# Performance work log

Hardware: AMD Instinct MI355X
Metric: run time of the kernel (lower is better)

## Reference

```python
import jax, jax.numpy as jnp
import numpy as np
from functools import partial

H = 128  # GRU hidden size
L = 16   # dim_latents


def _gru_dir(x_tbd, W_ih, W_hh, b_ih, b_hh):
    """Single-direction GRU over time-major input x_tbd [T,B,D] -> [T,B,H].
    Torch gate order: r, z, n."""
    T, B, _ = x_tbd.shape
    # Precompute input projections for all timesteps: [T,B,3H]
    xp = jnp.einsum('tbd,gd->tbg', x_tbd, W_ih) + b_ih
    h0 = jnp.zeros((B, H), dtype=x_tbd.dtype)

    def step(h, xp_t):
        gh = h @ W_hh.T + b_hh            # [B,3H]
        xr, xz, xn = jnp.split(xp_t, 3, axis=-1)
        hr, hz, hn = jnp.split(gh, 3, axis=-1)
        r = jax.nn.sigmoid(xr + hr)
        z = jax.nn.sigmoid(xz + hz)
        n = jnp.tanh(xn + r * hn)
        h_new = (1.0 - z) * n + z * h
        return h_new, h_new

    _, ys = jax.lax.scan(step, h0, xp)
    return ys  # [T,B,H]


def setup_inputs() -> dict:
    key = jax.random.key(0)
    ks = jax.random.split(key, 8)
    B, T, N = 256, 1000, 256
    s_ih = 1.0 / np.sqrt(N)
    s_hh = 1.0 / np.sqrt(H)
    s_fc = 1.0 / np.sqrt(2 * H + L)
    return {
        'y_aux': jax.random.normal(ks[0], (B, T, N), dtype=jnp.float32),
        'W_ih_fwd': jax.random.normal(ks[1], (3 * H, N), dtype=jnp.float32) * s_ih,
        'W_hh_fwd': jax.random.normal(ks[2], (3 * H, H), dtype=jnp.float32) * s_hh,
        'b_ih_fwd': jnp.zeros((3 * H,), dtype=jnp.float32),
        'b_hh_fwd': jnp.zeros((3 * H,), dtype=jnp.float32),
        'W_ih_bwd': jax.random.normal(ks[3], (3 * H, N), dtype=jnp.float32) * s_ih,
        'W_hh_bwd': jax.random.normal(ks[4], (3 * H, H), dtype=jnp.float32) * s_hh,
        'b_ih_bwd': jnp.zeros((3 * H,), dtype=jnp.float32),
        'b_hh_bwd': jnp.zeros((3 * H,), dtype=jnp.float32),
        'W_mu': jax.random.normal(ks[5], (L, 2 * H + L), dtype=jnp.float32) * s_fc,
        'b_mu': jnp.zeros((L,), dtype=jnp.float32),
        'W_lv': jax.random.normal(ks[6], (L, 2 * H + L), dtype=jnp.float32) * s_fc,
        'b_lv': jnp.zeros((L,), dtype=jnp.float32),
    }


def reference(y_aux, W_ih_fwd, W_hh_fwd, b_ih_fwd, b_hh_fwd,
              W_ih_bwd, W_hh_bwd, b_ih_bwd, b_hh_bwd,
              W_mu, b_mu, W_lv, b_lv):
    # [B,T,N] -> time-major [T,B,N]
    x = jnp.transpose(y_aux, (1, 0, 2))
    out_f = _gru_dir(x, W_ih_fwd, W_hh_fwd, b_ih_fwd, b_hh_fwd)
    out_b = _gru_dir(x[::-1], W_ih_bwd, W_hh_bwd, b_ih_bwd, b_hh_bwd)[::-1]
    rnn_output = jnp.concatenate([out_f, out_b], axis=-1)  # [T,B,2H]
    # hn[0]: bidirectional hidden states at t=0
    hn0 = rnn_output[0]                                    # [B,2H]
    B = hn0.shape[0]
    temp = jnp.concatenate([jnp.zeros((B, L), dtype=hn0.dtype), hn0], axis=1)
    mu_0 = temp @ W_mu.T + b_mu
    log_var_0 = temp @ W_lv.T + b_lv
    return (mu_0, log_var_0, rnn_output)
```

## Files before the change

### kernel.cpp

```cpp
#include <hip/hip_runtime.h>
#include <hip/hip_bf16.h>

typedef short bf16x8 __attribute__((ext_vector_type(8)));
typedef float f32x4  __attribute__((ext_vector_type(4)));

#define TSTEPS 1000
#define BATCH  256
#define NIN    256
#define HID    128
#define TC     40
#define LOG2E  1.44269504088896f

#define GIDX_N 8192
#define XP4_ELEMS (2ull*TSTEPS*GIDX_N)
#define XP2_OFF_BYTES (XP4_ELEMS*16ull)
#define XP_NEED (XP4_ELEMS*16ull + 2ull*TSTEPS*GIDX_N*8ull)

__device__ __forceinline__ ushort f2bf(float f){
  union { float f; unsigned u; } v; v.f = f;
  unsigned r = v.u + 0x7fffu + ((v.u >> 16) & 1u);
  return (ushort)(r >> 16);
}
__device__ __forceinline__ uint pk2(float lo, float hi){
  __hip_bfloat162 h = __float22bfloat162_rn(make_float2(lo, hi));
  union { __hip_bfloat162 h; uint u; } c; c.h = h; return c.u;
}
__device__ __forceinline__ float bflo(uint w){ union{uint u;float f;}c; c.u = w<<16; return c.f; }
__device__ __forceinline__ float bfhi(uint w){ union{uint u;float f;}c; c.u = w & 0xffff0000u; return c.f; }

__device__ __forceinline__ float sigmoid_fast(float x){
  return __builtin_amdgcn_rcpf(1.f + __expf(-x));
}
__device__ __forceinline__ float tanh_fast(float a){
  const float e = __expf(2.f*fabsf(a));
  const float t = fmaf(-2.f, __builtin_amdgcn_rcpf(e + 1.f), 1.f);
  return copysignf(t, a);
}
__device__ __forceinline__ bf16x8 ld_w8(const float* p){
  union { uint u[4]; bf16x8 v; } c;
  c.u[0]=pk2(p[0],p[1]); c.u[1]=pk2(p[2],p[3]);
  c.u[2]=pk2(p[4],p[5]); c.u[3]=pk2(p[6],p[7]);
  return c.v;
}
__device__ __forceinline__ bf16x8 ld_w8s(const float* p, float s){
  union { uint u[4]; bf16x8 v; } c;
  c.u[0]=pk2(p[0]*s,p[1]*s); c.u[1]=pk2(p[2]*s,p[3]*s);
  c.u[2]=pk2(p[4]*s,p[5]*s); c.u[3]=pk2(p[6]*s,p[7]*s);
  return c.v;
}

__global__ __launch_bounds__(512) void xp_gemm(
    const float* __restrict__ y_aux,
    const float* __restrict__ Wf, const float* __restrict__ bihf, const float* __restrict__ bhhf,
    const float* __restrict__ Wb, const float* __restrict__ bihb, const float* __restrict__ bhhb,
    uint4* __restrict__ xp4, uint2* __restrict__ xp2)
{
  const int nch = TSTEPS/TC;
  const int blk = blockIdx.x;
  const int dir = blk / (16*nch);
  const int rem = blk % (16*nch);
  const int btile = rem / nch;
  const int tch = rem % nch;
  const int b0 = btile*16;
  const int tid=threadIdx.x, wave=tid>>6, lane=tid&63, lrow=lane&15, lgrp=lane>>4;
  const float* Wih = dir? Wb : Wf;
  const float* bih = dir? bihb : bihf;
  const float* bhh = dir? bhhb : bhhf;

  __shared__ __align__(16) ushort xsh[2][16][264];

  bf16x8 wf[3][8];
  float biass[3];
  #pragma unroll
  for (int t3=0;t3<3;++t3){
    const int g = t3*128 + wave*16 + lrow;
    #pragma unroll
    for (int kk=0;kk<8;++kk)
      wf[t3][kk] = ld_w8(Wih + g*NIN + kk*32 + lgrp*8);
    biass[t3] = LOG2E * (bih[g] + (t3<2 ? bhh[g] : 0.f));
  }

  const int row = tid>>5, f8 = tid&31;
  const float* xsrc = y_aux + (size_t)(b0+row)*(TSTEPS*NIN) + (size_t)(tch*TC)*NIN + f8*8;
  {
    float4 a = *(const float4*)xsrc;
    float4 b = *(const float4*)(xsrc+4);
    union{uint u[4]; bf16x8 v;} c;
    c.u[0]=pk2(a.x,a.y); c.u[1]=pk2(a.z,a.w); c.u[2]=pk2(b.x,b.y); c.u[3]=pk2(b.z,b.w);
    *(bf16x8*)&xsh[0][row][f8*8] = c.v;
  }
  __syncthreads();

  const size_t gbase = ((size_t)dir*TSTEPS + (size_t)(tch*TC))*GIDX_N
                     + (size_t)((btile*8 + wave)*64 + lane);
  uint4* s4 = xp4 + gbase;
  uint2* s2 = xp2 + gbase;

  for (int k=0;k<TC;++k){
    const int cur=k&1, nxt=cur^1;
    const bool more = (k < TC-1);
    float4 pa, pb;
    if (more){
      const float* p = xsrc + (size_t)(k+1)*NIN;
      pa = *(const float4*)p;
      pb = *(const float4*)(p+4);
    }
    f32x4 a0={0,0,0,0}, a1={0,0,0,0}, a2={0,0,0,0};
    #pragma unroll
    for (int kk=0;kk<8;++kk){
      bf16x8 a = *(const bf16x8*)&xsh[cur][lrow][kk*32 + lgrp*8];
      a0 = __builtin_amdgcn_mfma_f32_16x16x32_bf16(a, wf[0][kk], a0, 0,0,0);
      a1 = __builtin_amdgcn_mfma_f32_16x16x32_bf16(a, wf[1][kk], a1, 0,0,0);
      a2 = __builtin_amdgcn_mfma_f32_16x16x32_bf16(a, wf[2][kk], a2, 0,0,0);
    }
    uint4 o4;
    o4.x = pk2(fmaf(LOG2E,a0[0],biass[0]), fmaf(LOG2E,a0[1],biass[0]));
    o4.y = pk2(fmaf(LOG2E,a0[2],biass[0]), fmaf(LOG2E,a0[3],biass[0]));
    o4.z = pk2(fmaf(LOG2E,a1[0],biass[1]), fmaf(LOG2E,a1[1],biass[1]));
    o4.w = pk2(fmaf(LOG2E,a1[2],biass[1]), fmaf(LOG2E,a1[3],biass[1]));
    uint2 o2;
    o2.x = pk2(fmaf(LOG2E,a2[0],biass[2]), fmaf(LOG2E,a2[1],biass[2]));
    o2.y = pk2(fmaf(LOG2E,a2[2],biass[2]), fmaf(LOG2E,a2[3],biass[2]));
    *s4 = o4;  s4 += GIDX_N;
    *s2 = o2;  s2 += GIDX_N;
    if (more){
      union{uint u[4]; bf16x8 v;} c;
      c.u[0]=pk2(pa.x,pa.y); c.u[1]=pk2(pa.z,pa.w); c.u[2]=pk2(pb.x,pb.y); c.u[3]=pk2(pb.z,pb.w);
      *(bf16x8*)&xsh[nxt][row][f8*8] = c.v;
    }
    asm volatile("s_waitcnt lgkmcnt(0)\n\ts_barrier" ::: "memory");
  }
}

__global__ __launch_bounds__(512) void gru_rec(
    const uint4* __restrict__ xp4, const uint2* __restrict__ xp2,
    const float* __restrict__ Whhf, const float* __restrict__ bhhf,
    const float* __restrict__ Whhb, const float* __restrict__ bhhb,
    float* __restrict__ out)
{
  const int blk=blockIdx.x, dir=blk>>4, btile=blk&15, b0=btile<<4;
  const int tid=threadIdx.x, wave=tid>>6, lane=tid&63, lrow=lane&15, lgrp=lane>>4;
  const float* Whh = dir? Whhb : Whhf;
  const float* bhh = dir? bhhb : bhhf;

  __shared__ __align__(16) ushort hbuf[2][16][136];

  bf16x8 whh[3][4];
  #pragma unroll
  for (int t3=0;t3<3;++t3){
    const int g = t3*128 + wave*16 + lrow;
    #pragma unroll
    for (int kk=0;kk<4;++kk)
      whh[t3][kk] = ld_w8s(Whh + g*HID + kk*32 + lgrp*8, LOG2E);
  }
  const int hcol = wave*16 + lrow;
  const float bh2s = LOG2E * bhh[256 + hcol];

  { ushort* hb=&hbuf[0][0][0]; for (int i=tid;i<16*136;i+=512) hb[i]=0; }

  const int tt0 = dir? (TSTEPS-1):0;
  const long long d4 = dir? -(long long)GIDX_N : (long long)GIDX_N;
  const size_t gbase = ((size_t)dir*TSTEPS + (size_t)tt0)*GIDX_N
                     + (size_t)((btile*8+wave)*64+lane);
  const uint4* q4p = xp4 + gbase;
  const uint2* q2p = xp2 + gbase;
  uint4 q40 = q4p[0], q41 = q4p[d4];
  uint2 q20 = q2p[0], q21 = q2p[d4];
  const uint4* f4 = q4p + 2*d4;
  const uint2* f2 = q2p + 2*d4;

  float* op = out + 8192 + (size_t)tt0*(BATCH*2*HID)
            + (size_t)(b0 + lgrp*4)*(2*HID) + dir*HID + hcol;
  const long long odel = dir? -(long long)(BATCH*2*HID) : (long long)(BATCH*2*HID);

  float hm[4]={0,0,0,0};
  __syncthreads();

  for (int s=0;s<TSTEPS;++s){
    const int cur=s&1, nxt=cur^1;
    uint4 q42 = *f4; f4 += d4;
    uint2 q22 = *f2; f2 += d4;

    f32x4 ar={0,0,0,0}, az={0,0,0,0}, an={0,0,0,0};
    #pragma unroll
    for (int kk=0;kk<4;++kk){
      bf16x8 a = *(const bf16x8*)&hbuf[cur][lrow][kk*32 + lgrp*8];
      ar = __builtin_amdgcn_mfma_f32_16x16x32_bf16(a, whh[0][kk], ar, 0,0,0);
      az = __builtin_amdgcn_mfma_f32_16x16x32_bf16(a, whh[1][kk], az, 0,0,0);
      an = __builtin_amdgcn_mfma_f32_16x16x32_bf16(a, whh[2][kk], an, 0,0,0);
    }

    float hv[4];
    {
      const float xr[4] = {bflo(q40.x),bfhi(q40.x),bflo(q40.y),bfhi(q40.y)};
      const float xz[4] = {bflo(q40.z),bfhi(q40.z),bflo(q40.w),bfhi(q40.w)};
      const float xn[4] = {bflo(q20.x),bfhi(q20.x),bflo(q20.y),bfhi(q20.y)};
      #pragma unroll
      for (int i=0;i<4;++i){
        const float r = __builtin_amdgcn_rcpf(1.f + __builtin_amdgcn_exp2f(-(ar[i]+xr[i])));
        const float z = __builtin_amdgcn_rcpf(1.f + __builtin_amdgcn_exp2f(-(az[i]+xz[i])));
        const float y  = fmaf(r, an[i]+bh2s, xn[i]);
        const float y2 = y + y;
        const float e  = __builtin_amdgcn_exp2f(fabsf(y2));
        const float t  = fmaf(-2.f, __builtin_amdgcn_rcpf(e+1.f), 1.f);
        const float n  = copysignf(t, y);
        hv[i] = fmaf(z, hm[i]-n, n);
        hm[i] = hv[i];
      }
    }
    const uint p01 = pk2(hv[0],hv[1]);
    const uint p23 = pk2(hv[2],hv[3]);
    hbuf[nxt][lgrp*4+0][hcol] = (ushort)p01;
    hbuf[nxt][lgrp*4+1][hcol] = (ushort)(p01>>16);
    hbuf[nxt][lgrp*4+2][hcol] = (ushort)p23;
    hbuf[nxt][lgrp*4+3][hcol] = (ushort)(p23>>16);
    op[0]   = hv[0];
    op[256] = hv[1];
    op[512] = hv[2];
    op[768] = hv[3];
    op += odel;
    q40=q41; q41=q42; q20=q21; q21=q22;
    asm volatile("s_waitcnt lgkmcnt(0)\n\ts_barrier" ::: "memory");
  }
}

__global__ __launch_bounds__(512) void gru_fused(
    const float* __restrict__ y_aux,
    const float* __restrict__ W_ih_f, const float* __restrict__ W_hh_f,
    const float* __restrict__ b_ih_f, const float* __restrict__ b_hh_f,
    const float* __restrict__ W_ih_b, const float* __restrict__ W_hh_b,
    const float* __restrict__ b_ih_b, const float* __restrict__ b_hh_b,
    float* __restrict__ out)
{
  const int blk  = blockIdx.x;
  const int dir  = blk >> 4;
  const int b0   = (blk & 15) << 4;
  const int tid  = threadIdx.x;
  const int wave = tid >> 6;
  const int lane = tid & 63;
  const int lrow = lane & 15;
  const int lgrp = lane >> 4;

  const float* Wih = dir ? W_ih_b : W_ih_f;
  const float* Whh = dir ? W_hh_b : W_hh_f;
  const float* bih = dir ? b_ih_b : b_ih_f;
  const float* bhh = dir ? b_hh_b : b_hh_f;

  __shared__ __align__(16) ushort hbuf[2][16][136];
  __shared__ __align__(16) ushort xbuf[2][16][264];

  bf16x8 wih_f[3][8];
  bf16x8 whh_f[3][4];
  #pragma unroll
  for (int t3 = 0; t3 < 3; ++t3){
    const int g = t3*128 + wave*16 + lrow;
    #pragma unroll
    for (int kk = 0; kk < 8; ++kk) wih_f[t3][kk] = ld_w8(Wih + g*NIN + kk*32 + lgrp*8);
    #pragma unroll
    for (int kk = 0; kk < 4; ++kk) whh_f[t3][kk] = ld_w8(Whh + g*HID + kk*32 + lgrp*8);
  }
  float bihv[3], bhhv[3];
  #pragma unroll
  for (int t3 = 0; t3 < 3; ++t3){
    const int g = t3*128 + wave*16 + lrow;
    bihv[t3] = bih[g];
    bhhv[t3] = bhh[g];
  }

  for (int i = tid; i < 2*16*136; i += 512) ((ushort*)hbuf)[i] = 0;
  {
    const int row = tid >> 5, f8 = tid & 31;
    const int t0  = dir ? (TSTEPS-1) : 0;
    const float* p = y_aux + (size_t)(b0+row)*(TSTEPS*NIN) + (size_t)t0*NIN + f8*8;
    union{uint u[4]; bf16x8 v;} c;
    float4 a = *(const float4*)p; float4 b = *(const float4*)(p+4);
    c.u[0]=pk2(a.x,a.y); c.u[1]=pk2(a.z,a.w); c.u[2]=pk2(b.x,b.y); c.u[3]=pk2(b.z,b.w);
    *(bf16x8*)&xbuf[0][row][f8*8] = c.v;
  }
  __syncthreads();

  float hm[4] = {0.f, 0.f, 0.f, 0.f};
  const int hcol = wave*16 + lrow;
  float* outr = out + 8192;

  for (int s = 0; s < TSTEPS; ++s){
    const int tt  = dir ? (TSTEPS-1-s) : s;
    const int cur = s & 1, nxt = cur ^ 1;
    const int tn   = dir ? (tt-1) : (tt+1);
    const int prow = tid >> 5, pf8 = tid & 31;
    const bool more = (s < TSTEPS-1);
    float4 pa, pb;
    if (more){
      const float* p = y_aux + (size_t)(b0+prow)*(TSTEPS*NIN) + (size_t)tn*NIN + pf8*8;
      pa = *(const float4*)p;
      pb = *(const float4*)(p+4);
    }

    f32x4 a_rh = {0,0,0,0}, a_zh = {0,0,0,0}, a_nh = {0,0,0,0};
    f32x4 a_rx = {0,0,0,0}, a_zx = {0,0,0,0}, a_nx = {0,0,0,0};
    #pragma unroll
    for (int kk = 0; kk < 4; ++kk){
      bf16x8 a = *(const bf16x8*)&hbuf[cur][lrow][kk*32 + lgrp*8];
      a_rh = __builtin_amdgcn_mfma_f32_16x16x32_bf16(a, whh_f[0][kk], a_rh, 0,0,0);
      a_zh = __builtin_amdgcn_mfma_f32_16x16x32_bf16(a, whh_f[1][kk], a_zh, 0,0,0);
      a_nh = __builtin_amdgcn_mfma_f32_16x16x32_bf16(a, whh_f[2][kk], a_nh, 0,0,0);
    }
    #pragma unroll
    for (int kk = 0; kk < 8; ++kk){
      bf16x8 a = *(const bf16x8*)&xbuf[cur][lrow][kk*32 + lgrp*8];
      a_rx = __builtin_amdgcn_mfma_f32_16x16x32_bf16(a, wih_f[0][kk], a_rx, 0,0,0);
      a_zx = __builtin_amdgcn_mfma_f32_16x16x32_bf16(a, wih_f[1][kk], a_zx, 0,0,0);
      a_nx = __builtin_amdgcn_mfma_f32_16x16x32_bf16(a, wih_f[2][kk], a_nx, 0,0,0);
    }

    #pragma unroll
    for (int i = 0; i < 4; ++i){
      const float rp  = a_rh[i] + a_rx[i] + bihv[0] + bhhv[0];
      const float zp  = a_zh[i] + a_zx[i] + bihv[1] + bhhv[1];
      const float hnp = a_nh[i] + bhhv[2];
      const float xnp = a_nx[i] + bihv[2];
      const float r = sigmoid_fast(rp);
      const float z = sigmoid_fast(zp);
      const float n = tanh_fast(fmaf(r, hnp, xnp));
      const float hv = n + z*(hm[i] - n);
      hm[i] = hv;
      outr[(size_t)tt*(BATCH*2*HID) + (size_t)(b0 + lgrp*4 + i)*(2*HID)
           + dir*HID + hcol] = hv;
      hbuf[nxt][lgrp*4 + i][hcol] = f2bf(hv);
    }

    if (more){
      union{uint u[4]; bf16x8 v;} c;
      c.u[0]=pk2(pa.x,pa.y); c.u[1]=pk2(pa.z,pa.w); c.u[2]=pk2(pb.x,pb.y); c.u[3]=pk2(pb.z,pb.w);
      *(bf16x8*)&xbuf[nxt][prow][pf8*8] = c.v;
    }
    __syncthreads();
  }
}

__global__ void heads(const float* __restrict__ out_rnn,
    const float* __restrict__ W_mu, const float* __restrict__ b_mu,
    const float* __restrict__ W_lv, const float* __restrict__ b_lv,
    float* __restrict__ out)
{
  const int oid   = blockIdx.x*256 + threadIdx.x;
  const int which = oid >> 12;
  const int r     = oid & 4095;
  const int b = r >> 4, j = r & 15;
  const float* W    = which ? W_lv : W_mu;
  const float* bias = which ? b_lv : b_mu;
  const float* h = out_rnn + b*256;
  const float* w = W + j*272 + 16;
  float acc = bias[j];
  for (int c = 0; c < 256; c += 4){
    acc += h[c]*w[c] + h[c+1]*w[c+1] + h[c+2]*w[c+2] + h[c+3]*w[c+3];
  }
  out[(which << 12) + r] = acc;
}

extern "C" void kernel_launch(void* const* d_in, const int* in_sizes, int n_in,
                              void* d_out, int out_size, void* d_ws, size_t ws_size,
                              hipStream_t stream)
{
  const float* y    = (const float*)d_in[0];
  const float* Wihf = (const float*)d_in[1];
  const float* Whhf = (const float*)d_in[2];
  const float* bihf = (const float*)d_in[3];
  const float* bhhf = (const float*)d_in[4];
  const float* Wihb = (const float*)d_in[5];
  const float* Whhb = (const float*)d_in[6];
  const float* bihb = (const float*)d_in[7];
  const float* bhhb = (const float*)d_in[8];
  const float* Wmu  = (const float*)d_in[9];
  const float* bmu  = (const float*)d_in[10];
  const float* Wlv  = (const float*)d_in[11];
  const float* blv  = (const float*)d_in[12];
  float* out = (float*)d_out;

  if (ws_size >= (size_t)XP_NEED){
    uint4* xp4 = (uint4*)d_ws;
    uint2* xp2 = (uint2*)((char*)d_ws + XP2_OFF_BYTES);
    xp_gemm<<<dim3(2*16*(TSTEPS/TC)), dim3(512), 0, stream>>>(
        y, Wihf, bihf, bhhf, Wihb, bihb, bhhb, xp4, xp2);
    gru_rec<<<dim3(32), dim3(512), 0, stream>>>(
        xp4, xp2, Whhf, bhhf, Whhb, bhhb, out);
  } else {
    gru_fused<<<dim3(32), dim3(512), 0, stream>>>(
        y, Wihf, Whhf, bihf, bhhf, Wihb, Whhb, bihb, bhhb, out);
  }
  heads<<<dim3(32), dim3(256), 0, stream>>>(out + 8192, Wmu, bmu, Wlv, blv, out);
}
```

Baseline: 958.7 us.

## Split GRU recurrence K dimension across wave pairs with LDS partial-sum exchange

The recurrent kernel now runs 1024 threads per block: each pair of waves splits the 128-wide hidden K dimension in half, exchanges partial MFMA sums through shared memory, and each wave finishes the gate math for two of the four rows. The aim is to halve the serial MFMA chain and the per-lane transcendental work on each timestep, which sit on the latency-bound critical path. The xp buffers are re-laid out so each half-wave pair reads its own two rows. This adds a second barrier and an LDS round trip per step, which may offset the savings.

```diff
diff --git a/kernel.cpp b/kernel.cpp
--- a/kernel.cpp
+++ b/kernel.cpp
@@ -11,10 +11,10 @@
 #define TC     40
 #define LOG2E  1.44269504088896f
 
-#define GIDX_N 8192
-#define XP4_ELEMS (2ull*TSTEPS*GIDX_N)
-#define XP2_OFF_BYTES (XP4_ELEMS*16ull)
-#define XP_NEED (XP4_ELEMS*16ull + 2ull*TSTEPS*GIDX_N*8ull)
+#define GIDX2_N 16384
+#define XPA_ELEMS (2ull*TSTEPS*GIDX2_N)
+#define XPB_OFF_BYTES (XPA_ELEMS*8ull)
+#define XP_NEED (XPA_ELEMS*8ull + XPA_ELEMS*4ull)
 
 __device__ __forceinline__ ushort f2bf(float f){
   union { float f; unsigned u; } v; v.f = f;
@@ -53,7 +53,7 @@
     const float* __restrict__ y_aux,
     const float* __restrict__ Wf, const float* __restrict__ bihf, const float* __restrict__ bhhf,
     const float* __restrict__ Wb, const float* __restrict__ bihb, const float* __restrict__ bhhb,
-    uint4* __restrict__ xp4, uint2* __restrict__ xp2)
+    uint2* __restrict__ xpA, uint* __restrict__ xpB)
 {
   const int nch = TSTEPS/TC;
   const int blk = blockIdx.x;
@@ -91,10 +91,8 @@
   }
   __syncthreads();
 
-  const size_t gbase = ((size_t)dir*TSTEPS + (size_t)(tch*TC))*GIDX_N
-                     + (size_t)((btile*8 + wave)*64 + lane);
-  uint4* s4 = xp4 + gbase;
-  uint2* s2 = xp2 + gbase;
+  size_t sidx = ((size_t)dir*TSTEPS + (size_t)(tch*TC))*GIDX2_N
+              + (size_t)(((btile*8 + wave)*2)*64 + lane);
 
   for (int k=0;k<TC;++k){
     const int cur=k&1, nxt=cur^1;
@@ -113,16 +111,19 @@
       a1 = __builtin_amdgcn_mfma_f32_16x16x32_bf16(a, wf[1][kk], a1, 0,0,0);
       a2 = __builtin_amdgcn_mfma_f32_16x16x32_bf16(a, wf[2][kk], a2, 0,0,0);
     }
-    uint4 o4;
-    o4.x = pk2(fmaf(LOG2E,a0[0],biass[0]), fmaf(LOG2E,a0[1],biass[0]));
-    o4.y = pk2(fmaf(LOG2E,a0[2],biass[0]), fmaf(LOG2E,a0[3],biass[0]));
-    o4.z = pk2(fmaf(LOG2E,a1[0],biass[1]), fmaf(LOG2E,a1[1],biass[1]));
-    o4.w = pk2(fmaf(LOG2E,a1[2],biass[1]), fmaf(LOG2E,a1[3],biass[1]));
-    uint2 o2;
-    o2.x = pk2(fmaf(LOG2E,a2[0],biass[2]), fmaf(LOG2E,a2[1],biass[2]));
-    o2.y = pk2(fmaf(LOG2E,a2[2],biass[2]), fmaf(LOG2E,a2[3],biass[2]));
-    *s4 = o4;  s4 += GIDX_N;
-    *s2 = o2;  s2 += GIDX_N;
+    const float r0=fmaf(LOG2E,a0[0],biass[0]), r1=fmaf(LOG2E,a0[1],biass[0]);
+    const float r2=fmaf(LOG2E,a0[2],biass[0]), r3=fmaf(LOG2E,a0[3],biass[0]);
+    const float z0=fmaf(LOG2E,a1[0],biass[1]), z1=fmaf(LOG2E,a1[1],biass[1]);
+    const float z2=fmaf(LOG2E,a1[2],biass[1]), z3=fmaf(LOG2E,a1[3],biass[1]);
+    const float n0=fmaf(LOG2E,a2[0],biass[2]), n1=fmaf(LOG2E,a2[1],biass[2]);
+    const float n2=fmaf(LOG2E,a2[2],biass[2]), n3=fmaf(LOG2E,a2[3],biass[2]);
+    uint2 qa0; qa0.x = pk2(r0,r1); qa0.y = pk2(z0,z1);
+    uint2 qa1; qa1.x = pk2(r2,r3); qa1.y = pk2(z2,z3);
+    xpA[sidx]    = qa0;
+    xpA[sidx+64] = qa1;
+    xpB[sidx]    = pk2(n0,n1);
+    xpB[sidx+64] = pk2(n2,n3);
+    sidx += GIDX2_N;
     if (more){
       union{uint u[4]; bf16x8 v;} c;
       c.u[0]=pk2(pa.x,pa.y); c.u[1]=pk2(pa.z,pa.w); c.u[2]=pk2(pb.x,pb.y); c.u[3]=pk2(pb.z,pb.w);
@@ -132,94 +133,121 @@
   }
 }
 
-__global__ __launch_bounds__(512) void gru_rec(
-    const uint4* __restrict__ xp4, const uint2* __restrict__ xp2,
+__global__ __launch_bounds__(1024) void gru_rec16(
+    const uint2* __restrict__ xpA, const uint* __restrict__ xpB,
     const float* __restrict__ Whhf, const float* __restrict__ bhhf,
     const float* __restrict__ Whhb, const float* __restrict__ bhhb,
     float* __restrict__ out)
 {
   const int blk=blockIdx.x, dir=blk>>4, btile=blk&15, b0=btile<<4;
   const int tid=threadIdx.x, wave=tid>>6, lane=tid&63, lrow=lane&15, lgrp=lane>>4;
+  const int g = wave>>1, kh = wave&1;
   const float* Whh = dir? Whhb : Whhf;
   const float* bhh = dir? bhhb : bhhf;
 
   __shared__ __align__(16) ushort hbuf[2][16][136];
-
-  bf16x8 whh[3][4];
+  __shared__ __align__(16) float rA[16][64][4];
+  __shared__ __align__(16) float rB[16][64][2];
+
+  bf16x8 whh[3][2];
   #pragma unroll
   for (int t3=0;t3<3;++t3){
-    const int g = t3*128 + wave*16 + lrow;
-    #pragma unroll
-    for (int kk=0;kk<4;++kk)
-      whh[t3][kk] = ld_w8s(Whh + g*HID + kk*32 + lgrp*8, LOG2E);
-  }
-  const int hcol = wave*16 + lrow;
+    const int gr = t3*128 + g*16 + lrow;
+    #pragma unroll
+    for (int kk=0;kk<2;++kk)
+      whh[t3][kk] = ld_w8s(Whh + gr*HID + kh*64 + kk*32 + lgrp*8, LOG2E);
+  }
+  const int hcol = g*16 + lrow;
   const float bh2s = LOG2E * bhh[256 + hcol];
-
-  { ushort* hb=&hbuf[0][0][0]; for (int i=tid;i<16*136;i+=512) hb[i]=0; }
+  const int oe = kh*2;
+  const int pe = 2 - oe;
+
+  { ushort* hb=&hbuf[0][0][0]; for (int i=tid;i<16*136;i+=1024) hb[i]=0; }
 
   const int tt0 = dir? (TSTEPS-1):0;
-  const long long d4 = dir? -(long long)GIDX_N : (long long)GIDX_N;
-  const size_t gbase = ((size_t)dir*TSTEPS + (size_t)tt0)*GIDX_N
-                     + (size_t)((btile*8+wave)*64+lane);
-  const uint4* q4p = xp4 + gbase;
-  const uint2* q2p = xp2 + gbase;
-  uint4 q40 = q4p[0], q41 = q4p[d4];
-  uint2 q20 = q2p[0], q21 = q2p[d4];
-  const uint4* f4 = q4p + 2*d4;
-  const uint2* f2 = q2p + 2*d4;
+  const long long dstep = dir? -(long long)GIDX2_N : (long long)GIDX2_N;
+  const size_t gb = ((size_t)dir*TSTEPS + (size_t)tt0)*GIDX2_N
+                  + (size_t)(((btile*8+g)*2+kh)*64 + lane);
+  const uint2* pAp = xpA + gb;
+  const uint*  pBp = xpB + gb;
+  uint2 qA0 = pAp[0], qA1 = pAp[dstep];
+  uint  qB0 = pBp[0], qB1 = pBp[dstep];
+  const uint2* fA = pAp + 2*dstep;
+  const uint*  fB = pBp + 2*dstep;
 
   float* op = out + 8192 + (size_t)tt0*(BATCH*2*HID)
-            + (size_t)(b0 + lgrp*4)*(2*HID) + dir*HID + hcol;
+            + (size_t)(b0 + lgrp*4 + oe)*(2*HID) + dir*HID + hcol;
   const long long odel = dir? -(long long)(BATCH*2*HID) : (long long)(BATCH*2*HID);
 
-  float hm[4]={0,0,0,0};
+  float hm0=0.f, hm1=0.f;
   __syncthreads();
 
   for (int s=0;s<TSTEPS;++s){
     const int cur=s&1, nxt=cur^1;
-    uint4 q42 = *f4; f4 += d4;
-    uint2 q22 = *f2; f2 += d4;
+    uint2 qA2 = *fA; fA += dstep;
+    uint  qB2 = *fB; fB += dstep;
 
     f32x4 ar={0,0,0,0}, az={0,0,0,0}, an={0,0,0,0};
-    #pragma unroll
-    for (int kk=0;kk<4;++kk){
-      bf16x8 a = *(const bf16x8*)&hbuf[cur][lrow][kk*32 + lgrp*8];
-      ar = __builtin_amdgcn_mfma_f32_16x16x32_bf16(a, whh[0][kk], ar, 0,0,0);
-      az = __builtin_amdgcn_mfma_f32_16x16x32_bf16(a, whh[1][kk], az, 0,0,0);
-      an = __builtin_amdgcn_mfma_f32_16x16x32_bf16(a, whh[2][kk], an, 0,0,0);
-    }
-
-    float hv[4];
     {
-      const float xr[4] = {bflo(q40.x),bfhi(q40.x),bflo(q40.y),bfhi(q40.y)};
-      const float xz[4] = {bflo(q40.z),bfhi(q40.z),bflo(q40.w),bfhi(q40.w)};
-      const float xn[4] = {bflo(q20.x),bfhi(q20.x),bflo(q20.y),bfhi(q20.y)};
-      #pragma unroll
-      for (int i=0;i<4;++i){
-        const float r = __builtin_amdgcn_rcpf(1.f + __builtin_amdgcn_exp2f(-(ar[i]+xr[i])));
-        const float z = __builtin_amdgcn_rcpf(1.f + __builtin_amdgcn_exp2f(-(az[i]+xz[i])));
-        const float y  = fmaf(r, an[i]+bh2s, xn[i]);
-        const float y2 = y + y;
-        const float e  = __builtin_amdgcn_exp2f(fabsf(y2));
-        const float t  = fmaf(-2.f, __builtin_amdgcn_rcpf(e+1.f), 1.f);
-        const float n  = copysignf(t, y);
-        hv[i] = fmaf(z, hm[i]-n, n);
-        hm[i] = hv[i];
-      }
-    }
-    const uint p01 = pk2(hv[0],hv[1]);
-    const uint p23 = pk2(hv[2],hv[3]);
-    hbuf[nxt][lgrp*4+0][hcol] = (ushort)p01;
-    hbuf[nxt][lgrp*4+1][hcol] = (ushort)(p01>>16);
-    hbuf[nxt][lgrp*4+2][hcol] = (ushort)p23;
-    hbuf[nxt][lgrp*4+3][hcol] = (ushort)(p23>>16);
-    op[0]   = hv[0];
-    op[256] = hv[1];
-    op[512] = hv[2];
-    op[768] = hv[3];
+      bf16x8 a0 = *(const bf16x8*)&hbuf[cur][lrow][kh*64 + lgrp*8];
+      bf16x8 a1 = *(const bf16x8*)&hbuf[cur][lrow][kh*64 + 32 + lgrp*8];
+      ar = __builtin_amdgcn_mfma_f32_16x16x32_bf16(a0, whh[0][0], ar, 0,0,0);
+      az = __builtin_amdgcn_mfma_f32_16x16x32_bf16(a0, whh[1][0], az, 0,0,0);
+      an = __builtin_amdgcn_mfma_f32_16x16x32_bf16(a0, whh[2][0], an, 0,0,0);
+      ar = __builtin_amdgcn_mfma_f32_16x16x32_bf16(a1, whh[0][1], ar, 0,0,0);
+      az = __builtin_amdgcn_mfma_f32_16x16x32_bf16(a1, whh[1][1], az, 0,0,0);
+      an = __builtin_amdgcn_mfma_f32_16x16x32_bf16(a1, whh[2][1], an, 0,0,0);
+    }
+
+    f32x4 w4; w4[0]=ar[pe]; w4[1]=ar[pe+1]; w4[2]=az[pe]; w4[3]=az[pe+1];
+    *(f32x4*)&rA[wave][lane][0] = w4;
+    float2 w2; w2.x=an[pe]; w2.y=an[pe+1];
+    *(float2*)&rB[wave][lane][0] = w2;
+    asm volatile("s_waitcnt lgkmcnt(0)\n\ts_barrier" ::: "memory");
+
+    const f32x4 p4 = *(const f32x4*)&rA[wave^1][lane][0];
+    const float2 p2 = *(const float2*)&rB[wave^1][lane][0];
+    const float R0 = ar[oe]   + p4[0];
+    const float R1 = ar[oe+1] + p4[1];
+    const float Z0 = az[oe]   + p4[2];
+    const float Z1 = az[oe+1] + p4[3];
+    const float N0 = an[oe]   + p2.x;
+    const float N1 = an[oe+1] + p2.y;
+
+    const float xr0=bflo(qA0.x), xr1=bfhi(qA0.x);
+    const float xz0=bflo(qA0.y), xz1=bfhi(qA0.y);
+    const float xn0=bflo(qB0),   xn1=bfhi(qB0);
+
+    float hv0, hv1;
+    {
+      const float r = __builtin_amdgcn_rcpf(1.f + __builtin_amdgcn_exp2f(-(R0+xr0)));
+      const float z = __builtin_amdgcn_rcpf(1.f + __builtin_amdgcn_exp2f(-(Z0+xz0)));
+      const float y  = fmaf(r, N0+bh2s, xn0);
+      const float y2 = y + y;
+      const float e  = __builtin_amdgcn_exp2f(fabsf(y2));
+      const float t  = fmaf(-2.f, __builtin_amdgcn_rcpf(e+1.f), 1.f);
+      const float n  = copysignf(t, y);
+      hv0 = fmaf(z, hm0-n, n);  hm0 = hv0;
+    }
+    {
+      const float r = __builtin_amdgcn_rcpf(1.f + __builtin_amdgcn_exp2f(-(R1+xr1)));
+      const float z = __builtin_amdgcn_rcpf(1.f + __builtin_amdgcn_exp2f(-(Z1+xz1)));
+      const float y  = fmaf(r, N1+bh2s, xn1);
+      const float y2 = y + y;
+      const float e  = __builtin_amdgcn_exp2f(fabsf(y2));
+      const float t  = fmaf(-2.f, __builtin_amdgcn_rcpf(e+1.f), 1.f);
+      const float n  = copysignf(t, y);
+      hv1 = fmaf(z, hm1-n, n);  hm1 = hv1;
+    }
+
+    op[0]   = hv0;
+    op[256] = hv1;
+    const uint p01 = pk2(hv0, hv1);
+    hbuf[nxt][lgrp*4+oe  ][hcol] = (ushort)p01;
+    hbuf[nxt][lgrp*4+oe+1][hcol] = (ushort)(p01>>16);
+
     op += odel;
-    q40=q41; q41=q42; q20=q21; q21=q22;
+    qA0=qA1; qA1=qA2; qB0=qB1; qB1=qB2;
     asm volatile("s_waitcnt lgkmcnt(0)\n\ts_barrier" ::: "memory");
   }
 }
@@ -378,12 +406,12 @@
   float* out = (float*)d_out;
 
   if (ws_size >= (size_t)XP_NEED){
-    uint4* xp4 = (uint4*)d_ws;
-    uint2* xp2 = (uint2*)((char*)d_ws + XP2_OFF_BYTES);
+    uint2* xpA = (uint2*)d_ws;
+    uint*  xpB = (uint*)((char*)d_ws + XPB_OFF_BYTES);
     xp_gemm<<<dim3(2*16*(TSTEPS/TC)), dim3(512), 0, stream>>>(
-        y, Wihf, bihf, bhhf, Wihb, bihb, bhhb, xp4, xp2);
-    gru_rec<<<dim3(32), dim3(512), 0, stream>>>(
-        xp4, xp2, Whhf, bhhf, Whhb, bhhb, out);
+        y, Wihf, bihf, bhhf, Wihb, bihb, bhhb, xpA, xpB);
+    gru_rec16<<<dim3(32), dim3(1024), 0, stream>>>(
+        xpA, xpB, Whhf, bhhf, Whhb, bhhb, out);
   } else {
     gru_fused<<<dim3(32), dim3(512), 0, stream>>>(
         y, Wihf, Whhf, bihf, bhhf, Wihb, Whhb, bihb, bhhb, out);
```

New measurement: 1.319 ms. 1.38x slower.

## Fuse input-projection GEMM and GRU recurrence into one kernel with flag-based chunk pipelining

Applied to the files above, without the earlier changes.

Merges the separate xp_gemm and gru_rec launches into one kernel. The first 32 blocks run the recurrence and the remaining blocks compute input projections in time chunks, ordered so that chunks needed early are produced first. Each producer block publishes a per-chunk release flag, and the recurrent blocks spin on the next chunk's flag before consuming it, so the recurrence can start before the whole GEMM finishes. It also folds LOG2E into the weights and seeds the accumulators with the bias, and halves the chunk size. This depends on the recurrent blocks being co-resident with the producers and adds spin-wait, flag-reset memset and fence overhead.

```diff
diff --git a/kernel.cpp b/kernel.cpp
--- a/kernel.cpp
+++ b/kernel.cpp
@@ -8,13 +8,17 @@
 #define BATCH  256
 #define NIN    256
 #define HID    128
-#define TC     40
+#define TC     20
+#define NCH    50
 #define LOG2E  1.44269504088896f
 
 #define GIDX_N 8192
 #define XP4_ELEMS (2ull*TSTEPS*GIDX_N)
 #define XP2_OFF_BYTES (XP4_ELEMS*16ull)
-#define XP_NEED (XP4_ELEMS*16ull + 2ull*TSTEPS*GIDX_N*8ull)
+#define FLAGS_OFF (XP4_ELEMS*16ull + XP4_ELEMS*8ull)
+#define NFLAGS (2*16*NCH)
+#define FLAG_BYTES (NFLAGS*4)
+#define WS_NEED (FLAGS_OFF + (unsigned long long)FLAG_BYTES)
 
 __device__ __forceinline__ ushort f2bf(float f){
   union { float f; unsigned u; } v; v.f = f;
@@ -49,101 +53,104 @@
   return c.v;
 }
 
-__global__ __launch_bounds__(512) void xp_gemm(
+__global__ __launch_bounds__(512, 2) void vae_fused(
     const float* __restrict__ y_aux,
-    const float* __restrict__ Wf, const float* __restrict__ bihf, const float* __restrict__ bhhf,
-    const float* __restrict__ Wb, const float* __restrict__ bihb, const float* __restrict__ bhhb,
-    uint4* __restrict__ xp4, uint2* __restrict__ xp2)
-{
-  const int nch = TSTEPS/TC;
-  const int blk = blockIdx.x;
-  const int dir = blk / (16*nch);
-  const int rem = blk % (16*nch);
-  const int btile = rem / nch;
-  const int tch = rem % nch;
-  const int b0 = btile*16;
-  const int tid=threadIdx.x, wave=tid>>6, lane=tid&63, lrow=lane&15, lgrp=lane>>4;
-  const float* Wih = dir? Wb : Wf;
-  const float* bih = dir? bihb : bihf;
-  const float* bhh = dir? bhhb : bhhf;
-
-  __shared__ __align__(16) ushort xsh[2][16][264];
-
-  bf16x8 wf[3][8];
-  float biass[3];
-  #pragma unroll
-  for (int t3=0;t3<3;++t3){
-    const int g = t3*128 + wave*16 + lrow;
-    #pragma unroll
-    for (int kk=0;kk<8;++kk)
-      wf[t3][kk] = ld_w8(Wih + g*NIN + kk*32 + lgrp*8);
-    biass[t3] = LOG2E * (bih[g] + (t3<2 ? bhh[g] : 0.f));
-  }
-
-  const int row = tid>>5, f8 = tid&31;
-  const float* xsrc = y_aux + (size_t)(b0+row)*(TSTEPS*NIN) + (size_t)(tch*TC)*NIN + f8*8;
-  {
-    float4 a = *(const float4*)xsrc;
-    float4 b = *(const float4*)(xsrc+4);
-    union{uint u[4]; bf16x8 v;} c;
-    c.u[0]=pk2(a.x,a.y); c.u[1]=pk2(a.z,a.w); c.u[2]=pk2(b.x,b.y); c.u[3]=pk2(b.z,b.w);
-    *(bf16x8*)&xsh[0][row][f8*8] = c.v;
-  }
-  __syncthreads();
-
-  const size_t gbase = ((size_t)dir*TSTEPS + (size_t)(tch*TC))*GIDX_N
-                     + (size_t)((btile*8 + wave)*64 + lane);
-  uint4* s4 = xp4 + gbase;
-  uint2* s2 = xp2 + gbase;
-
-  for (int k=0;k<TC;++k){
-    const int cur=k&1, nxt=cur^1;
-    const bool more = (k < TC-1);
-    float4 pa, pb;
-    if (more){
-      const float* p = xsrc + (size_t)(k+1)*NIN;
-      pa = *(const float4*)p;
-      pb = *(const float4*)(p+4);
-    }
-    f32x4 a0={0,0,0,0}, a1={0,0,0,0}, a2={0,0,0,0};
-    #pragma unroll
-    for (int kk=0;kk<8;++kk){
-      bf16x8 a = *(const bf16x8*)&xsh[cur][lrow][kk*32 + lgrp*8];
-      a0 = __builtin_amdgcn_mfma_f32_16x16x32_bf16(a, wf[0][kk], a0, 0,0,0);
-      a1 = __builtin_amdgcn_mfma_f32_16x16x32_bf16(a, wf[1][kk], a1, 0,0,0);
-      a2 = __builtin_amdgcn_mfma_f32_16x16x32_bf16(a, wf[2][kk], a2, 0,0,0);
-    }
-    uint4 o4;
-    o4.x = pk2(fmaf(LOG2E,a0[0],biass[0]), fmaf(LOG2E,a0[1],biass[0]));
-    o4.y = pk2(fmaf(LOG2E,a0[2],biass[0]), fmaf(LOG2E,a0[3],biass[0]));
-    o4.z = pk2(fmaf(LOG2E,a1[0],biass[1]), fmaf(LOG2E,a1[1],biass[1]));
-    o4.w = pk2(fmaf(LOG2E,a1[2],biass[1]), fmaf(LOG2E,a1[3],biass[1]));
-    uint2 o2;
-    o2.x = pk2(fmaf(LOG2E,a2[0],biass[2]), fmaf(LOG2E,a2[1],biass[2]));
-    o2.y = pk2(fmaf(LOG2E,a2[2],biass[2]), fmaf(LOG2E,a2[3],biass[2]));
-    *s4 = o4;  s4 += GIDX_N;
-    *s2 = o2;  s2 += GIDX_N;
-    if (more){
-      union{uint u[4]; bf16x8 v;} c;
-      c.u[0]=pk2(pa.x,pa.y); c.u[1]=pk2(pa.z,pa.w); c.u[2]=pk2(pb.x,pb.y); c.u[3]=pk2(pb.z,pb.w);
-      *(bf16x8*)&xsh[nxt][row][f8*8] = c.v;
-    }
-    asm volatile("s_waitcnt lgkmcnt(0)\n\ts_barrier" ::: "memory");
-  }
-}
-
-__global__ __launch_bounds__(512) void gru_rec(
-    const uint4* __restrict__ xp4, const uint2* __restrict__ xp2,
-    const float* __restrict__ Whhf, const float* __restrict__ bhhf,
-    const float* __restrict__ Whhb, const float* __restrict__ bhhb,
+    const float* __restrict__ Wihf, const float* __restrict__ bihf, const float* __restrict__ bhhf,
+    const float* __restrict__ Wihb, const float* __restrict__ bihb, const float* __restrict__ bhhb,
+    const float* __restrict__ Whhf, const float* __restrict__ Whhb,
+    uint4* __restrict__ xp4, uint2* __restrict__ xp2,
+    uint* __restrict__ flags,
     float* __restrict__ out)
 {
+  __shared__ __align__(16) union {
+    ushort xsh[2][16][264];
+    ushort hbuf[2][16][136];
+  } sm;
+
+  const int tid=threadIdx.x, wave=tid>>6, lane=tid&63, lrow=lane&15, lgrp=lane>>4;
+
+  if (blockIdx.x >= 32){
+    const int pb   = blockIdx.x - 32;
+    const int pr   = pb >> 5;
+    const int sub  = pb & 31;
+    const int dir  = sub >> 4;
+    const int btile= sub & 15;
+    const int tch  = dir ? (NCH-1-pr) : pr;
+    const int b0   = btile*16;
+    const float* Wih = dir? Wihb : Wihf;
+    const float* bih = dir? bihb : bihf;
+    const float* bhh = dir? bhhb : bhhf;
+
+    bf16x8 wf[3][8];
+    f32x4 cinit[3];
+    #pragma unroll
+    for (int t3=0;t3<3;++t3){
+      const int g = t3*128 + wave*16 + lrow;
+      #pragma unroll
+      for (int kk=0;kk<8;++kk)
+        wf[t3][kk] = ld_w8s(Wih + g*NIN + kk*32 + lgrp*8, LOG2E);
+      const float bv = LOG2E * (bih[g] + (t3<2 ? bhh[g] : 0.f));
+      cinit[t3][0]=bv; cinit[t3][1]=bv; cinit[t3][2]=bv; cinit[t3][3]=bv;
+    }
+
+    const int row = tid>>5, f8 = tid&31;
+    const float* xsrc = y_aux + (size_t)(b0+row)*(TSTEPS*NIN)
+                      + (size_t)(tch*TC)*NIN + f8*8;
+    {
+      float4 a = *(const float4*)xsrc;
+      float4 b = *(const float4*)(xsrc+4);
+      union{uint u[4]; bf16x8 v;} c;
+      c.u[0]=pk2(a.x,a.y); c.u[1]=pk2(a.z,a.w); c.u[2]=pk2(b.x,b.y); c.u[3]=pk2(b.z,b.w);
+      *(bf16x8*)&sm.xsh[0][row][f8*8] = c.v;
+    }
+    __syncthreads();
+
+    size_t sidx = ((size_t)dir*TSTEPS + (size_t)(tch*TC))*GIDX_N
+                + (size_t)((btile*8 + wave)*64 + lane);
+
+    for (int k=0;k<TC;++k){
+      const int cur=k&1, nxt=cur^1;
+      const bool more = (k < TC-1);
+      float4 pa, pb2;
+      if (more){
+        const float* p = xsrc + (size_t)(k+1)*NIN;
+        pa  = *(const float4*)p;
+        pb2 = *(const float4*)(p+4);
+      }
+      f32x4 a0=cinit[0], a1=cinit[1], a2=cinit[2];
+      #pragma unroll
+      for (int kk=0;kk<8;++kk){
+        bf16x8 a = *(const bf16x8*)&sm.xsh[cur][lrow][kk*32 + lgrp*8];
+        a0 = __builtin_amdgcn_mfma_f32_16x16x32_bf16(a, wf[0][kk], a0, 0,0,0);
+        a1 = __builtin_amdgcn_mfma_f32_16x16x32_bf16(a, wf[1][kk], a1, 0,0,0);
+        a2 = __builtin_amdgcn_mfma_f32_16x16x32_bf16(a, wf[2][kk], a2, 0,0,0);
+      }
+      uint4 o4; o4.x=pk2(a0[0],a0[1]); o4.y=pk2(a0[2],a0[3]);
+                o4.z=pk2(a1[0],a1[1]); o4.w=pk2(a1[2],a1[3]);
+      uint2 o2; o2.x=pk2(a2[0],a2[1]); o2.y=pk2(a2[2],a2[3]);
+      xp4[sidx]=o4; xp2[sidx]=o2; sidx += GIDX_N;
+      if (more){
+        union{uint u[4]; bf16x8 v;} c;
+        c.u[0]=pk2(pa.x,pa.y); c.u[1]=pk2(pa.z,pa.w);
+        c.u[2]=pk2(pb2.x,pb2.y); c.u[3]=pk2(pb2.z,pb2.w);
+        *(bf16x8*)&sm.xsh[nxt][row][f8*8] = c.v;
+      }
+      asm volatile("s_waitcnt lgkmcnt(0)\n\ts_barrier" ::: "memory");
+    }
+
+    __threadfence();
+    __syncthreads();
+    if (tid==0){
+      __hip_atomic_store(&flags[(dir*16 + btile)*NCH + tch], 1u,
+                         __ATOMIC_RELEASE, __HIP_MEMORY_SCOPE_AGENT);
+    }
+    return;
+  }
+
   const int blk=blockIdx.x, dir=blk>>4, btile=blk&15, b0=btile<<4;
-  const int tid=threadIdx.x, wave=tid>>6, lane=tid&63, lrow=lane&15, lgrp=lane>>4;
   const float* Whh = dir? Whhb : Whhf;
   const float* bhh = dir? bhhb : bhhf;
-
-  __shared__ __align__(16) ushort hbuf[2][16][136];
+  const uint* fbase = flags + (dir*16 + btile)*NCH;
 
   bf16x8 whh[3][4];
   #pragma unroll
@@ -156,7 +163,17 @@
   const int hcol = wave*16 + lrow;
   const float bh2s = LOG2E * bhh[256 + hcol];
 
-  { ushort* hb=&hbuf[0][0][0]; for (int i=tid;i<16*136;i+=512) hb[i]=0; }
+  { ushort* hb=&sm.hbuf[0][0][0]; for (int i=tid;i<16*136;i+=512) hb[i]=0; }
+
+  {
+    const int c0 = dir ? (NCH-1) : 0;
+    if (tid==0){
+      while (__hip_atomic_load(&fbase[c0], __ATOMIC_ACQUIRE,
+                               __HIP_MEMORY_SCOPE_AGENT) == 0u)
+        __builtin_amdgcn_s_sleep(2);
+    }
+    __syncthreads();
+  }
 
   const int tt0 = dir? (TSTEPS-1):0;
   const long long d4 = dir? -(long long)GIDX_N : (long long)GIDX_N;
@@ -174,53 +191,63 @@
   const long long odel = dir? -(long long)(BATCH*2*HID) : (long long)(BATCH*2*HID);
 
   float hm[4]={0,0,0,0};
-  __syncthreads();
-
-  for (int s=0;s<TSTEPS;++s){
-    const int cur=s&1, nxt=cur^1;
-    uint4 q42 = *f4; f4 += d4;
-    uint2 q22 = *f2; f2 += d4;
-
-    f32x4 ar={0,0,0,0}, az={0,0,0,0}, an={0,0,0,0};
-    #pragma unroll
-    for (int kk=0;kk<4;++kk){
-      bf16x8 a = *(const bf16x8*)&hbuf[cur][lrow][kk*32 + lgrp*8];
-      ar = __builtin_amdgcn_mfma_f32_16x16x32_bf16(a, whh[0][kk], ar, 0,0,0);
-      az = __builtin_amdgcn_mfma_f32_16x16x32_bf16(a, whh[1][kk], az, 0,0,0);
-      an = __builtin_amdgcn_mfma_f32_16x16x32_bf16(a, whh[2][kk], an, 0,0,0);
-    }
-
-    float hv[4];
-    {
-      const float xr[4] = {bflo(q40.x),bfhi(q40.x),bflo(q40.y),bfhi(q40.y)};
-      const float xz[4] = {bflo(q40.z),bfhi(q40.z),bflo(q40.w),bfhi(q40.w)};
-      const float xn[4] = {bflo(q20.x),bfhi(q20.x),bflo(q20.y),bfhi(q20.y)};
+
+  for (int ch=0; ch<NCH; ++ch){
+    if (ch+1 < NCH){
+      const int cn = dir ? (NCH-2-ch) : (ch+1);
+      if (tid==0){
+        while (__hip_atomic_load(&fbase[cn], __ATOMIC_ACQUIRE,
+                                 __HIP_MEMORY_SCOPE_AGENT) == 0u)
+          __builtin_amdgcn_s_sleep(2);
+      }
+      __syncthreads();
+    }
+    for (int k=0;k<TC;++k){
+      const int cur=k&1, nxt=cur^1;
+      uint4 q42 = *f4; f4 += d4;
+      uint2 q22 = *f2; f2 += d4;
+
+      f32x4 ar={0,0,0,0}, az={0,0,0,0}, an={0,0,0,0};
       #pragma unroll
-      for (int i=0;i<4;++i){
-        const float r = __builtin_amdgcn_rcpf(1.f + __builtin_amdgcn_exp2f(-(ar[i]+xr[i])));
-        const float z = __builtin_amdgcn_rcpf(1.f + __builtin_amdgcn_exp2f(-(az[i]+xz[i])));
-        const float y  = fmaf(r, an[i]+bh2s, xn[i]);
-        const float y2 = y + y;
-        const float e  = __builtin_amdgcn_exp2f(fabsf(y2));
-        const float t  = fmaf(-2.f, __builtin_amdgcn_rcpf(e+1.f), 1.f);
-        const float n  = copysignf(t, y);
-        hv[i] = fmaf(z, hm[i]-n, n);
-        hm[i] = hv[i];
-      }
-    }
-    const uint p01 = pk2(hv[0],hv[1]);
-    const uint p23 = pk2(hv[2],hv[3]);
-    hbuf[nxt][lgrp*4+0][hcol] = (ushort)p01;
-    hbuf[nxt][lgrp*4+1][hcol] = (ushort)(p01>>16);
-    hbuf[nxt][lgrp*4+2][hcol] = (ushort)p23;
-    hbuf[nxt][lgrp*4+3][hcol] = (ushort)(p23>>16);
-    op[0]   = hv[0];
-    op[256] = hv[1];
-    op[512] = hv[2];
-    op[768] = hv[3];
-    op += odel;
-    q40=q41; q41=q42; q20=q21; q21=q22;
-    asm volatile("s_waitcnt lgkmcnt(0)\n\ts_barrier" ::: "memory");
+      for (int kk=0;kk<4;++kk){
+        bf16x8 a = *(const bf16x8*)&sm.hbuf[cur][lrow][kk*32 + lgrp*8];
+        ar = __builtin_amdgcn_mfma_f32_16x16x32_bf16(a, whh[0][kk], ar, 0,0,0);
+        az = __builtin_amdgcn_mfma_f32_16x16x32_bf16(a, whh[1][kk], az, 0,0,0);
+        an = __builtin_amdgcn_mfma_f32_16x16x32_bf16(a, whh[2][kk], an, 0,0,0);
+      }
+
+      float hv[4];
+      {
+        const float xr[4] = {bflo(q40.x),bfhi(q40.x),bflo(q40.y),bfhi(q40.y)};
+        const float xz[4] = {bflo(q40.z),bfhi(q40.z),bflo(q40.w),bfhi(q40.w)};
+        const float xn[4] = {bflo(q20.x),bfhi(q20.x),bflo(q20.y),bfhi(q20.y)};
+        #pragma unroll
+        for (int i=0;i<4;++i){
+          const float r = __builtin_amdgcn_rcpf(1.f + __builtin_amdgcn_exp2f(-(ar[i]+xr[i])));
+          const float z = __builtin_amdgcn_rcpf(1.f + __builtin_amdgcn_exp2f(-(az[i]+xz[i])));
+          const float y  = fmaf(r, an[i]+bh2s, xn[i]);
+          const float y2 = y + y;
+          const float e  = __builtin_amdgcn_exp2f(fabsf(y2));
+          const float t  = fmaf(-2.f, __builtin_amdgcn_rcpf(e+1.f), 1.f);
+          const float n  = copysignf(t, y);
+          hv[i] = fmaf(z, hm[i]-n, n);
+          hm[i] = hv[i];
+        }
+      }
+      const uint p01 = pk2(hv[0],hv[1]);
+      const uint p23 = pk2(hv[2],hv[3]);
+      sm.hbuf[nxt][lgrp*4+0][hcol] = (ushort)p01;
+      sm.hbuf[nxt][lgrp*4+1][hcol] = (ushort)(p01>>16);
+      sm.hbuf[nxt][lgrp*4+2][hcol] = (ushort)p23;
+      sm.hbuf[nxt][lgrp*4+3][hcol] = (ushort)(p23>>16);
+      op[0]   = hv[0];
+      op[256] = hv[1];
+      op[512] = hv[2];
+      op[768] = hv[3];
+      op += odel;
+      q40=q41; q41=q42; q20=q21; q21=q22;
+      asm volatile("s_waitcnt lgkmcnt(0)\n\ts_barrier" ::: "memory");
+    }
   }
 }
 
@@ -377,13 +404,14 @@
   const float* blv  = (const float*)d_in[12];
   float* out = (float*)d_out;
 
-  if (ws_size >= (size_t)XP_NEED){
-    uint4* xp4 = (uint4*)d_ws;
-    uint2* xp2 = (uint2*)((char*)d_ws + XP2_OFF_BYTES);
-    xp_gemm<<<dim3(2*16*(TSTEPS/TC)), dim3(512), 0, stream>>>(
-        y, Wihf, bihf, bhhf, Wihb, bihb, bhhb, xp4, xp2);
-    gru_rec<<<dim3(32), dim3(512), 0, stream>>>(
-        xp4, xp2, Whhf, bhhf, Whhb, bhhb, out);
+  if (ws_size >= (size_t)WS_NEED){
+    uint4* xp4  = (uint4*)d_ws;
+    uint2* xp2  = (uint2*)((char*)d_ws + XP2_OFF_BYTES);
+    uint* flags = (uint*)((char*)d_ws + FLAGS_OFF);
+    hipMemsetAsync(flags, 0, FLAG_BYTES, stream);
+    vae_fused<<<dim3(32 + 2*16*NCH), dim3(512), 0, stream>>>(
+        y, Wihf, bihf, bhhf, Wihb, bihb, bhhb, Whhf, Whhb,
+        xp4, xp2, flags, out);
   } else {
     gru_fused<<<dim3(32), dim3(512), 0, stream>>>(
         y, Wihf, Whhf, bihf, bhhf, Wihb, Whhb, bihb, bhhb, out);
```

Result: slower. 1.380 ms (+43.9%).
